# Kernel optimization log

Measured on AMD Instinct MI355X. Metric: run time of the kernel, lower is better.

The kernel has to match this reference:

```python
import jax, jax.numpy as jnp
import numpy as np

LSH_NUM_PROJS = 7
BLOCK_SIZE = 256
SAMPLE_SIZE = 256
B, H, N, D = 2, 16, 8192, 64


def _gray_perm(num_projs):
    # Gray-code ordering so adjacent hash buckets differ by 1 bit (AngularLSH.perm)
    a = np.array([0, 1], dtype=np.int32)
    for _ in range(num_projs - 1):
        a = np.concatenate([a, a[::-1] + a.shape[0]])
    return a

_PERM = jnp.asarray(_gray_perm(LSH_NUM_PROJS))
_ENC = 2 ** jnp.arange(LSH_NUM_PROJS, dtype=jnp.int32)


def lsh_hash(x, proj_dir):
    # x: [b,h,n,d], proj_dir: [1,1,d,r] -> bucket ids [b,h,n]
    proj = jnp.einsum('...nd,...dr->...nr', x, proj_dir)
    bits = (proj > 0).astype(jnp.int32)
    return _PERM[(bits * _ENC).sum(-1)]


def gather_seq(x, idx):
    # x: [b,h,n,d], idx: [b,h,s] -> [b,h,s,d]
    return jnp.take_along_axis(x, idx[..., None], axis=2)


def setup_inputs() -> dict:
    key = jax.random.key(0)
    kq, kk, kv, kp, ks = jax.random.split(key, 5)
    query = jax.random.normal(kq, (B, H, N, D), dtype=jnp.float32)
    key_t = jax.random.normal(kk, (B, H, N, D), dtype=jnp.float32)
    value = jax.random.normal(kv, (B, H, N, D), dtype=jnp.float32)
    proj_dir = jax.random.normal(kp, (1, 1, D, LSH_NUM_PROJS), dtype=jnp.float32)
    # uniform sampling WITHOUT replacement per (b,h), like torch.multinomial
    skeys = jax.random.split(ks, B * H)
    sampled_set = jax.vmap(lambda k: jax.random.permutation(k, N)[:SAMPLE_SIZE])(skeys)
    sampled_set = sampled_set.reshape(B, H, SAMPLE_SIZE).astype(jnp.int32)
    return {'query': query, 'key': key_t, 'value': value,
            'proj_dir': proj_dir, 'sampled_set': sampled_set}


def reference(query, key, value, proj_dir, sampled_set):
    b, h, n, d = query.shape
    scale = d ** -0.5
    neg_min = jnp.finfo(query.dtype).min

    # ---- 1. LSH-sort queries and keys (stable sort on bucket ids) ----
    q_idx = jnp.argsort(lsh_hash(query, proj_dir), axis=2, stable=True)
    k_idx = jnp.argsort(lsh_hash(key, proj_dir), axis=2, stable=True)
    q_idx_inv = jnp.argsort(q_idx, axis=2, stable=True)
    q_s = gather_seq(query, q_idx)
    k_s = gather_seq(key, k_idx)
    v_s = gather_seq(value, k_idx)

    # ---- 2. block-diagonal exact attention on sorted order ----
    nb = n // BLOCK_SIZE               # n divisible by block_size (8192/256=32)
    qbs = n // nb                       # query_block_size == 256 here
    qb = q_s.reshape(b, h, nb, qbs, d)
    kb = k_s.reshape(b, h, nb, BLOCK_SIZE, d)
    vb = v_s.reshape(b, h, nb, BLOCK_SIZE, d)
    qk = jnp.einsum('bhnqd,bhnkd->bhnqk', qb, kb) * scale
    lse_blk = jax.nn.logsumexp(qk, axis=-1, keepdims=True)
    attn_blk = jnp.einsum('bhnqk,bhnkd->bhnqd', jnp.exp(qk - lse_blk), vb)
    attn_blk = attn_blk.reshape(b, h, n, d)
    lse_blk = lse_blk.reshape(b, h, n, 1)

    # ---- 3. sampled-column residual attention ----
    k_sub = gather_seq(k_s, sampled_set)   # [b,h,S,d]
    v_sub = gather_seq(v_s, sampled_set)
    row_blk = (jnp.arange(n) // qbs)[None, None, :, None]            # [1,1,n,1]
    col_blk = (sampled_set // BLOCK_SIZE)[:, :, None, :]             # [b,h,1,S]
    in_block = row_blk == col_blk                                    # [b,h,n,S]
    sampled_cnt = SAMPLE_SIZE - in_block.sum(-1, keepdims=True).astype(query.dtype)
    bias = in_block.astype(query.dtype) * neg_min                    # mask double-counted cols
    qk_r = jnp.einsum('bhnd,bhsd->bhns', q_s, k_sub) * scale + bias
    lse_r = jax.nn.logsumexp(qk_r, axis=-1, keepdims=True)
    attn_r = jnp.einsum('bhns,bhsd->bhnd', jnp.exp(qk_r - lse_r), v_sub)
    # approximate_unsampled: rescale sampled mass to stand in for all
    # (n - block_size) out-of-block columns
    lse_r = lse_r + jnp.log((n - BLOCK_SIZE) / sampled_cnt)

    # ---- 4. combine the two attention estimates (add_self_attentions) ----
    lse = jnp.logaddexp(lse_blk, lse_r)
    c = jnp.exp(lse_blk - lse)
    attn = c * attn_blk + (1.0 - c) * attn_r

    # ---- 5. un-sort rows back to original query order ----
    attn = gather_seq(attn, q_idx_inv)
    return attn
```

## Files before the change

kernel.cpp:

```cpp
#include <hip/hip_runtime.h>
#include <math.h>

#define BH    32
#define NSEQ  8192
#define DDIM  64
#define NPROJ 7
#define BLK   256
#define NB    32
#define PITCH 72
#define PPITCH 40
#define LOG2E 1.44269504f
#define SC2   0.180336881f

typedef _Float16 v8h __attribute__((ext_vector_type(8)));
typedef _Float16 v4h __attribute__((ext_vector_type(4)));
typedef float    v4f __attribute__((ext_vector_type(4)));

__global__ __launch_bounds__(256) void hash_kernel(
        const float* __restrict__ query,
        const float* __restrict__ key,
        const float* __restrict__ proj,
        int* __restrict__ buckets)
{
    const float* x = (blockIdx.y == 0) ? query : key;
    const int t = threadIdx.x;
    const int row = blockIdx.x * 256 + t;

    __shared__ double pdd[64 * NPROJ];
    for (int i = t; i < 64 * NPROJ; i += 256) pdd[i] = (double)proj[i];
    __syncthreads();

    const float4* rp = (const float4*)(x + (size_t)row * DDIM);
    double acc[NPROJ];
    #pragma unroll
    for (int r = 0; r < NPROJ; ++r) acc[r] = 0.0;

    #pragma unroll
    for (int i = 0; i < 16; ++i) {
        float4 v = rp[i];
        float e[4] = {v.x, v.y, v.z, v.w};
        #pragma unroll
        for (int c = 0; c < 4; ++c) {
            double xv = (double)e[c];
            const int d = i * 4 + c;
            #pragma unroll
            for (int r = 0; r < NPROJ; ++r)
                acc[r] += xv * pdd[d * NPROJ + r];
        }
    }
    int code = 0;
    #pragma unroll
    for (int r = 0; r < NPROJ; ++r)
        if (acc[r] > 0.0) code |= (1 << r);
    buckets[(size_t)blockIdx.y * (BH * NSEQ) + row] = code ^ (code >> 1);
}

#define SCNT 258
__global__ __launch_bounds__(256) void sort_kernel(
        const int* __restrict__ buckets,
        int* __restrict__ q_idx,
        int* __restrict__ k_idx)
{
    const int bh = blockIdx.x;
    const int t = threadIdx.x;
    const int lane = t & 63, w = t >> 6;
    const int* b = buckets + (size_t)blockIdx.y * (BH * NSEQ) + (size_t)bh * NSEQ;
    int* out = ((blockIdx.y == 0) ? q_idx : k_idx) + (size_t)bh * NSEQ;

    __shared__ unsigned short cnt[128 * SCNT];
    __shared__ unsigned int partial[256];
    __shared__ unsigned int wsum[4];

    unsigned int* cz = (unsigned int*)cnt;
    for (int i = t; i < 128 * SCNT / 2; i += 256) cz[i] = 0;

    int4 rv[8];
    const int4* b4 = (const int4*)b;
    #pragma unroll
    for (int s = 0; s < 8; ++s) rv[s] = b4[t * 8 + s];
    __syncthreads();

    #pragma unroll
    for (int s = 0; s < 8; ++s) {
        cnt[rv[s].x * SCNT + t]++;
        cnt[rv[s].y * SCNT + t]++;
        cnt[rv[s].z * SCNT + t]++;
        cnt[rv[s].w * SCNT + t]++;
    }
    __syncthreads();

    const int v0 = t >> 1, tt0 = (t & 1) * 128;
    {
        unsigned int s = 0;
        for (int j = 0; j < 128; ++j) s += cnt[v0 * SCNT + tt0 + j];
        partial[t] = s;
    }
    __syncthreads();

    unsigned int chunkoff;
    {
        unsigned int x = partial[t], own = x;
        #pragma unroll
        for (int d = 1; d < 64; d <<= 1) {
            unsigned int y = __shfl_up(x, d);
            if (lane >= d) x += y;
        }
        if (lane == 63) wsum[w] = x;
        __syncthreads();
        unsigned int wb0 = 0;
        if (w == 1) wb0 = wsum[0];
        else if (w == 2) wb0 = wsum[0] + wsum[1];
        else if (w == 3) wb0 = wsum[0] + wsum[1] + wsum[2];
        chunkoff = x - own + wb0;
    }

    {
        unsigned int s = chunkoff;
        for (int j = 0; j < 128; ++j) {
            unsigned short c = cnt[v0 * SCNT + tt0 + j];
            cnt[v0 * SCNT + tt0 + j] = (unsigned short)s;
            s += c;
        }
    }
    __syncthreads();

    const int i0 = t * 32;
    #pragma unroll
    for (int s = 0; s < 8; ++s) {
        int4 q = rv[s];
        int j4 = i0 + s * 4;
        { unsigned short p = cnt[q.x * SCNT + t]++; out[p] = j4 + 0; }
        { unsigned short p = cnt[q.y * SCNT + t]++; out[p] = j4 + 1; }
        { unsigned short p = cnt[q.z * SCNT + t]++; out[p] = j4 + 2; }
        { unsigned short p = cnt[q.w * SCNT + t]++; out[p] = j4 + 3; }
    }
}

__global__ __launch_bounds__(256, 2) void attn_kernel(
        const float* __restrict__ query,
        const float* __restrict__ key,
        const float* __restrict__ value,
        const int* __restrict__ sampled,
        const int* __restrict__ q_idx,
        const int* __restrict__ k_idx,
        float* __restrict__ outp)
{
    const int qb = blockIdx.x;
    const int bh = blockIdx.y;
    const int t  = threadIdx.x;
    const int w    = t >> 6;
    const int lane = t & 63;
    const int quad = lane >> 4;
    const int nrow = lane & 15;

    __shared__ __align__(16) unsigned char smem[38912];
    _Float16* Kc = (_Float16*)smem;
    _Float16* Vt = (_Float16*)(smem + 9216);
    _Float16* Pb = (_Float16*)(smem + 18432);
    _Float16* Ob = (_Float16*)smem;
    __shared__ int s_row[512];
    __shared__ __align__(16) float lb[512];
    __shared__ int s_qi[256];
    __shared__ int wb[4];

    const size_t bhN = (size_t)bh * NSEQ;

    {
        s_qi[t] = q_idx[bhN + qb * BLK + t];
        s_row[t] = k_idx[bhN + qb * BLK + t];
        int ss = sampled[bh * BLK + t];
        s_row[256 + t] = k_idx[bhN + ss];
        int sb = ss >> 8;
        unsigned long long mk = __ballot(sb == qb);
        if (lane == 0) wb[w] = __popcll(mk);
        __syncthreads();
        int cnt_in = wb[0] + wb[1] + wb[2] + wb[3];
        float J = __logf((float)(NSEQ - BLK) / (float)(BLK - cnt_in));
        lb[t] = -6.0f * LOG2E;
        lb[256 + t] = (sb == qb) ? -3.0e4f : (J - 6.0f) * LOG2E;
    }

    const int kr_r = t >> 2, kr_seg = t & 3;
    const int vs_kq = t & 15, vs_dg = t >> 4;

    float4 kreg0, kreg1, kreg2, kreg3;
    float4 vreg0, vreg1, vreg2, vreg3;

    #define ISSUE_LOADS(ch_) do {                                              \
        int krow_ = s_row[(ch_) * 64 + kr_r];                                  \
        const float4* kp_ = (const float4*)(key + (bhN + (size_t)krow_) * DDIM \
                                            + kr_seg * 16);                    \
        kreg0 = kp_[0]; kreg1 = kp_[1]; kreg2 = kp_[2]; kreg3 = kp_[3];        \
        int vr0_ = s_row[(ch_) * 64 + vs_kq * 4 + 0];                          \
        int vr1_ = s_row[(ch_) * 64 + vs_kq * 4 + 1];                          \
        int vr2_ = s_row[(ch_) * 64 + vs_kq * 4 + 2];                          \
        int vr3_ = s_row[(ch_) * 64 + vs_kq * 4 + 3];                          \
        vreg0 = *(const float4*)(value + (bhN + (size_t)vr0_) * DDIM + vs_dg * 4); \
        vreg1 = *(const float4*)(value + (bhN + (size_t)vr1_) * DDIM + vs_dg * 4); \
        vreg2 = *(const float4*)(value + (bhN + (size_t)vr2_) * DDIM + vs_dg * 4); \
        vreg3 = *(const float4*)(value + (bhN + (size_t)vr3_) * DDIM + vs_dg * 4); \
    } while (0)

    ISSUE_LOADS(0);

    v8h qf[4][2];
    #pragma unroll
    for (int ni = 0; ni < 4; ++ni) {
        int qi = s_qi[w * 64 + ni * 16 + nrow];
        const float* qp = query + (bhN + (size_t)qi) * DDIM;
        #pragma unroll
        for (int k2 = 0; k2 < 2; ++k2) {
            const float4* q4 = (const float4*)(qp + k2 * 32 + quad * 8);
            float4 a = q4[0], bvec = q4[1];
            v8h h;
            h[0]=(_Float16)a.x; h[1]=(_Float16)a.y; h[2]=(_Float16)a.z; h[3]=(_Float16)a.w;
            h[4]=(_Float16)bvec.x; h[5]=(_Float16)bvec.y; h[6]=(_Float16)bvec.z; h[7]=(_Float16)bvec.w;
            qf[ni][k2] = h;
        }
    }

    v4f Oacc[4][4];
    float l_part[4];
    #pragma unroll
    for (int ni = 0; ni < 4; ++ni) {
        l_part[ni] = 0.f;
        #pragma unroll
        for (int mi2 = 0; mi2 < 4; ++mi2) Oacc[mi2][ni] = (v4f){0.f, 0.f, 0.f, 0.f};
    }
    _Float16* Pw = Pb + w * 64 * PPITCH;

    #pragma unroll 1
    for (int ch = 0; ch < 8; ++ch) {
        __syncthreads();
        {
            v8h h0, h1;
            h0[0]=(_Float16)kreg0.x; h0[1]=(_Float16)kreg0.y; h0[2]=(_Float16)kreg0.z; h0[3]=(_Float16)kreg0.w;
            h0[4]=(_Float16)kreg1.x; h0[5]=(_Float16)kreg1.y; h0[6]=(_Float16)kreg1.z; h0[7]=(_Float16)kreg1.w;
            h1[0]=(_Float16)kreg2.x; h1[1]=(_Float16)kreg2.y; h1[2]=(_Float16)kreg2.z; h1[3]=(_Float16)kreg2.w;
            h1[4]=(_Float16)kreg3.x; h1[5]=(_Float16)kreg3.y; h1[6]=(_Float16)kreg3.z; h1[7]=(_Float16)kreg3.w;
            *(v8h*)&Kc[kr_r * PITCH + kr_seg * 16] = h0;
            *(v8h*)&Kc[kr_r * PITCH + kr_seg * 16 + 8] = h1;
        }
        {
            v4h h0, h1, h2, h3;
            h0[0]=(_Float16)vreg0.x; h0[1]=(_Float16)vreg1.x; h0[2]=(_Float16)vreg2.x; h0[3]=(_Float16)vreg3.x;
            h1[0]=(_Float16)vreg0.y; h1[1]=(_Float16)vreg1.y; h1[2]=(_Float16)vreg2.y; h1[3]=(_Float16)vreg3.y;
            h2[0]=(_Float16)vreg0.z; h2[1]=(_Float16)vreg1.z; h2[2]=(_Float16)vreg2.z; h2[3]=(_Float16)vreg3.z;
            h3[0]=(_Float16)vreg0.w; h3[1]=(_Float16)vreg1.w; h3[2]=(_Float16)vreg2.w; h3[3]=(_Float16)vreg3.w;
            *(v4h*)&Vt[(vs_dg * 4 + 0) * PITCH + vs_kq * 4] = h0;
            *(v4h*)&Vt[(vs_dg * 4 + 1) * PITCH + vs_kq * 4] = h1;
            *(v4h*)&Vt[(vs_dg * 4 + 2) * PITCH + vs_kq * 4] = h2;
            *(v4h*)&Vt[(vs_dg * 4 + 3) * PITCH + vs_kq * 4] = h3;
        }
        if (ch < 7) ISSUE_LOADS(ch + 1);
        __syncthreads();

        #pragma unroll
        for (int ks = 0; ks < 2; ++ks) {
            #pragma unroll
            for (int mi = 0; mi < 2; ++mi) {
                v4f bb = *(const v4f*)&lb[ch * 64 + ks * 32 + mi * 16 + quad * 4];
                const int krow = ks * 32 + mi * 16 + nrow;
                v8h ka0 = *(const v8h*)&Kc[krow * PITCH + quad * 8];
                v8h ka1 = *(const v8h*)&Kc[krow * PITCH + 32 + quad * 8];
                #pragma unroll
                for (int ni = 0; ni < 4; ++ni) {
                    v4f S = (v4f){0.f, 0.f, 0.f, 0.f};
                    S = __builtin_amdgcn_mfma_f32_16x16x32_f16(ka0, qf[ni][0], S, 0, 0, 0);
                    S = __builtin_amdgcn_mfma_f32_16x16x32_f16(ka1, qf[ni][1], S, 0, 0, 0);
                    v4h ph;
                    #pragma unroll
                    for (int r = 0; r < 4; ++r)
                        ph[r] = (_Float16)__builtin_amdgcn_exp2f(fmaf(S[r], SC2, bb[r]));
                    l_part[ni] += ((float)ph[0] + (float)ph[1])
                                + ((float)ph[2] + (float)ph[3]);
                    *(v4h*)&Pw[(ni * 16 + nrow) * PPITCH + mi * 16 + quad * 4] = ph;
                }
            }
            v8h pbv[4];
            #pragma unroll
            for (int ni = 0; ni < 4; ++ni)
                pbv[ni] = *(const v8h*)&Pw[(ni * 16 + nrow) * PPITCH + quad * 8];
            __builtin_amdgcn_s_setprio(1);
            #pragma unroll
            for (int mi2 = 0; mi2 < 4; ++mi2) {
                v8h va = *(const v8h*)&Vt[(mi2 * 16 + nrow) * PITCH + ks * 32 + quad * 8];
                #pragma unroll
                for (int ni = 0; ni < 4; ++ni)
                    Oacc[mi2][ni] = __builtin_amdgcn_mfma_f32_16x16x32_f16(va, pbv[ni], Oacc[mi2][ni], 0, 0, 0);
            }
            __builtin_amdgcn_s_setprio(0);
        }
    }

    __syncthreads();
    #pragma unroll
    for (int ni = 0; ni < 4; ++ni) {
        float l = l_part[ni];
        l += __shfl_xor(l, 16);
        l += __shfl_xor(l, 32);
        float inv = 1.0f / l;
        #pragma unroll
        for (int mi2 = 0; mi2 < 4; ++mi2) {
            v4h h;
            #pragma unroll
            for (int r = 0; r < 4; ++r)
                h[r] = (_Float16)(Oacc[mi2][ni][r] * inv);
            *(v4h*)&Ob[(w * 64 + ni * 16 + nrow) * PITCH + mi2 * 16 + quad * 4] = h;
        }
    }
    __syncthreads();

    #pragma unroll
    for (int p = 0; p < 4; ++p) {
        int row = p * 64 + (t >> 2);
        int seg = t & 3;
        const _Float16* src = &Ob[row * PITCH + seg * 16];
        v8h x0 = *(const v8h*)src;
        v8h x1 = *(const v8h*)(src + 8);
        int qi = s_qi[row];
        float4* op = (float4*)(outp + (bhN + (size_t)qi) * DDIM + seg * 16);
        op[0] = make_float4((float)x0[0], (float)x0[1], (float)x0[2], (float)x0[3]);
        op[1] = make_float4((float)x0[4], (float)x0[5], (float)x0[6], (float)x0[7]);
        op[2] = make_float4((float)x1[0], (float)x1[1], (float)x1[2], (float)x1[3]);
        op[3] = make_float4((float)x1[4], (float)x1[5], (float)x1[6], (float)x1[7]);
    }
}

extern "C" void kernel_launch(void* const* d_in, const int* in_sizes, int n_in,
                              void* d_out, int out_size, void* d_ws, size_t ws_size,
                              hipStream_t stream) {
    (void)in_sizes; (void)n_in; (void)out_size; (void)ws_size;
    const float* query = (const float*)d_in[0];
    const float* key   = (const float*)d_in[1];
    const float* value = (const float*)d_in[2];
    const float* proj  = (const float*)d_in[3];
    const int* sampled = (const int*)d_in[4];
    float* out = (float*)d_out;

    int* buckets = (int*)d_ws;
    int* q_idx   = buckets + 2 * BH * NSEQ;
    int* k_idx   = q_idx + BH * NSEQ;

    hash_kernel<<<dim3(BH * NSEQ / 256, 2), 256, 0, stream>>>(query, key, proj, buckets);
    sort_kernel<<<dim3(BH, 2), 256, 0, stream>>>(buckets, q_idx, k_idx);
    attn_kernel<<<dim3(NB, BH), 256, 0, stream>>>(query, key, value, sampled,
                                                  q_idx, k_idx, out);
}
```

Baseline: 290.3 us.

## Split attention block across eight waves with fewer query rows each

Doubles the attention block size from 256 to 512 threads so each wave handles 32 query rows instead of 64. The K/V staging work is redistributed so each thread loads half as much. The goal is fewer registers per thread and more waves to hide latency. The tighter launch bound (512 threads, 4 blocks) may force register spills, and each wave now does less MFMA work per shared-memory read.

```diff
diff --git a/kernel.cpp b/kernel.cpp
--- a/kernel.cpp
+++ b/kernel.cpp
@@ -136,7 +136,7 @@
     }
 }
 
-__global__ __launch_bounds__(256, 2) void attn_kernel(
+__global__ __launch_bounds__(512, 4) void attn_kernel(
         const float* __restrict__ query,
         const float* __restrict__ key,
         const float* __restrict__ value,
@@ -165,48 +165,51 @@
 
     const size_t bhN = (size_t)bh * NSEQ;
 
-    {
+    int ss = 0, sb = 0;
+    if (t < 256) {
         s_qi[t] = q_idx[bhN + qb * BLK + t];
         s_row[t] = k_idx[bhN + qb * BLK + t];
-        int ss = sampled[bh * BLK + t];
+        ss = sampled[bh * BLK + t];
         s_row[256 + t] = k_idx[bhN + ss];
-        int sb = ss >> 8;
+        sb = ss >> 8;
         unsigned long long mk = __ballot(sb == qb);
         if (lane == 0) wb[w] = __popcll(mk);
-        __syncthreads();
+    }
+    __syncthreads();
+    if (t < 256) {
         int cnt_in = wb[0] + wb[1] + wb[2] + wb[3];
         float J = __logf((float)(NSEQ - BLK) / (float)(BLK - cnt_in));
         lb[t] = -6.0f * LOG2E;
         lb[256 + t] = (sb == qb) ? -3.0e4f : (J - 6.0f) * LOG2E;
     }
 
-    const int kr_r = t >> 2, kr_seg = t & 3;
+    const int kr_r = t >> 3, kr_seg = t & 7;
     const int vs_kq = t & 15, vs_dg = t >> 4;
 
-    float4 kreg0, kreg1, kreg2, kreg3;
-    float4 vreg0, vreg1, vreg2, vreg3;
+    float4 kreg0, kreg1;
+    float2 vreg0, vreg1, vreg2, vreg3;
 
     #define ISSUE_LOADS(ch_) do {                                              \
         int krow_ = s_row[(ch_) * 64 + kr_r];                                  \
         const float4* kp_ = (const float4*)(key + (bhN + (size_t)krow_) * DDIM \
-                                            + kr_seg * 16);                    \
-        kreg0 = kp_[0]; kreg1 = kp_[1]; kreg2 = kp_[2]; kreg3 = kp_[3];        \
+                                            + kr_seg * 8);                     \
+        kreg0 = kp_[0]; kreg1 = kp_[1];                                        \
         int vr0_ = s_row[(ch_) * 64 + vs_kq * 4 + 0];                          \
         int vr1_ = s_row[(ch_) * 64 + vs_kq * 4 + 1];                          \
         int vr2_ = s_row[(ch_) * 64 + vs_kq * 4 + 2];                          \
         int vr3_ = s_row[(ch_) * 64 + vs_kq * 4 + 3];                          \
-        vreg0 = *(const float4*)(value + (bhN + (size_t)vr0_) * DDIM + vs_dg * 4); \
-        vreg1 = *(const float4*)(value + (bhN + (size_t)vr1_) * DDIM + vs_dg * 4); \
-        vreg2 = *(const float4*)(value + (bhN + (size_t)vr2_) * DDIM + vs_dg * 4); \
-        vreg3 = *(const float4*)(value + (bhN + (size_t)vr3_) * DDIM + vs_dg * 4); \
+        vreg0 = *(const float2*)(value + (bhN + (size_t)vr0_) * DDIM + vs_dg * 2); \
+        vreg1 = *(const float2*)(value + (bhN + (size_t)vr1_) * DDIM + vs_dg * 2); \
+        vreg2 = *(const float2*)(value + (bhN + (size_t)vr2_) * DDIM + vs_dg * 2); \
+        vreg3 = *(const float2*)(value + (bhN + (size_t)vr3_) * DDIM + vs_dg * 2); \
     } while (0)
 
     ISSUE_LOADS(0);
 
-    v8h qf[4][2];
-    #pragma unroll
-    for (int ni = 0; ni < 4; ++ni) {
-        int qi = s_qi[w * 64 + ni * 16 + nrow];
+    v8h qf[2][2];
+    #pragma unroll
+    for (int ni = 0; ni < 2; ++ni) {
+        int qi = s_qi[w * 32 + ni * 16 + nrow];
         const float* qp = query + (bhN + (size_t)qi) * DDIM;
         #pragma unroll
         for (int k2 = 0; k2 < 2; ++k2) {
@@ -219,38 +222,31 @@
         }
     }
 
-    v4f Oacc[4][4];
-    float l_part[4];
-    #pragma unroll
-    for (int ni = 0; ni < 4; ++ni) {
+    v4f Oacc[4][2];
+    float l_part[2];
+    #pragma unroll
+    for (int ni = 0; ni < 2; ++ni) {
         l_part[ni] = 0.f;
         #pragma unroll
         for (int mi2 = 0; mi2 < 4; ++mi2) Oacc[mi2][ni] = (v4f){0.f, 0.f, 0.f, 0.f};
     }
-    _Float16* Pw = Pb + w * 64 * PPITCH;
+    _Float16* Pw = Pb + w * 32 * PPITCH;
 
     #pragma unroll 1
     for (int ch = 0; ch < 8; ++ch) {
         __syncthreads();
         {
-            v8h h0, h1;
+            v8h h0;
             h0[0]=(_Float16)kreg0.x; h0[1]=(_Float16)kreg0.y; h0[2]=(_Float16)kreg0.z; h0[3]=(_Float16)kreg0.w;
             h0[4]=(_Float16)kreg1.x; h0[5]=(_Float16)kreg1.y; h0[6]=(_Float16)kreg1.z; h0[7]=(_Float16)kreg1.w;
-            h1[0]=(_Float16)kreg2.x; h1[1]=(_Float16)kreg2.y; h1[2]=(_Float16)kreg2.z; h1[3]=(_Float16)kreg2.w;
-            h1[4]=(_Float16)kreg3.x; h1[5]=(_Float16)kreg3.y; h1[6]=(_Float16)kreg3.z; h1[7]=(_Float16)kreg3.w;
-            *(v8h*)&Kc[kr_r * PITCH + kr_seg * 16] = h0;
-            *(v8h*)&Kc[kr_r * PITCH + kr_seg * 16 + 8] = h1;
+            *(v8h*)&Kc[kr_r * PITCH + kr_seg * 8] = h0;
         }
         {
-            v4h h0, h1, h2, h3;
+            v4h h0, h1;
             h0[0]=(_Float16)vreg0.x; h0[1]=(_Float16)vreg1.x; h0[2]=(_Float16)vreg2.x; h0[3]=(_Float16)vreg3.x;
             h1[0]=(_Float16)vreg0.y; h1[1]=(_Float16)vreg1.y; h1[2]=(_Float16)vreg2.y; h1[3]=(_Float16)vreg3.y;
-            h2[0]=(_Float16)vreg0.z; h2[1]=(_Float16)vreg1.z; h2[2]=(_Float16)vreg2.z; h2[3]=(_Float16)vreg3.z;
-            h3[0]=(_Float16)vreg0.w; h3[1]=(_Float16)vreg1.w; h3[2]=(_Float16)vreg2.w; h3[3]=(_Float16)vreg3.w;
-            *(v4h*)&Vt[(vs_dg * 4 + 0) * PITCH + vs_kq * 4] = h0;
-            *(v4h*)&Vt[(vs_dg * 4 + 1) * PITCH + vs_kq * 4] = h1;
-            *(v4h*)&Vt[(vs_dg * 4 + 2) * PITCH + vs_kq * 4] = h2;
-            *(v4h*)&Vt[(vs_dg * 4 + 3) * PITCH + vs_kq * 4] = h3;
+            *(v4h*)&Vt[(vs_dg * 2 + 0) * PITCH + vs_kq * 4] = h0;
+            *(v4h*)&Vt[(vs_dg * 2 + 1) * PITCH + vs_kq * 4] = h1;
         }
         if (ch < 7) ISSUE_LOADS(ch + 1);
         __syncthreads();
@@ -264,7 +260,7 @@
                 v8h ka0 = *(const v8h*)&Kc[krow * PITCH + quad * 8];
                 v8h ka1 = *(const v8h*)&Kc[krow * PITCH + 32 + quad * 8];
                 #pragma unroll
-                for (int ni = 0; ni < 4; ++ni) {
+                for (int ni = 0; ni < 2; ++ni) {
                     v4f S = (v4f){0.f, 0.f, 0.f, 0.f};
                     S = __builtin_amdgcn_mfma_f32_16x16x32_f16(ka0, qf[ni][0], S, 0, 0, 0);
                     S = __builtin_amdgcn_mfma_f32_16x16x32_f16(ka1, qf[ni][1], S, 0, 0, 0);
@@ -277,16 +273,16 @@
                     *(v4h*)&Pw[(ni * 16 + nrow) * PPITCH + mi * 16 + quad * 4] = ph;
                 }
             }
-            v8h pbv[4];
-            #pragma unroll
-            for (int ni = 0; ni < 4; ++ni)
+            v8h pbv[2];
+            #pragma unroll
+            for (int ni = 0; ni < 2; ++ni)
                 pbv[ni] = *(const v8h*)&Pw[(ni * 16 + nrow) * PPITCH + quad * 8];
             __builtin_amdgcn_s_setprio(1);
             #pragma unroll
             for (int mi2 = 0; mi2 < 4; ++mi2) {
                 v8h va = *(const v8h*)&Vt[(mi2 * 16 + nrow) * PITCH + ks * 32 + quad * 8];
                 #pragma unroll
-                for (int ni = 0; ni < 4; ++ni)
+                for (int ni = 0; ni < 2; ++ni)
                     Oacc[mi2][ni] = __builtin_amdgcn_mfma_f32_16x16x32_f16(va, pbv[ni], Oacc[mi2][ni], 0, 0, 0);
             }
             __builtin_amdgcn_s_setprio(0);
@@ -295,7 +291,7 @@
 
     __syncthreads();
     #pragma unroll
-    for (int ni = 0; ni < 4; ++ni) {
+    for (int ni = 0; ni < 2; ++ni) {
         float l = l_part[ni];
         l += __shfl_xor(l, 16);
         l += __shfl_xor(l, 32);
@@ -306,14 +302,14 @@
             #pragma unroll
             for (int r = 0; r < 4; ++r)
                 h[r] = (_Float16)(Oacc[mi2][ni][r] * inv);
-            *(v4h*)&Ob[(w * 64 + ni * 16 + nrow) * PITCH + mi2 * 16 + quad * 4] = h;
-        }
-    }
-    __syncthreads();
-
-    #pragma unroll
-    for (int p = 0; p < 4; ++p) {
-        int row = p * 64 + (t >> 2);
+            *(v4h*)&Ob[(w * 32 + ni * 16 + nrow) * PITCH + mi2 * 16 + quad * 4] = h;
+        }
+    }
+    __syncthreads();
+
+    #pragma unroll
+    for (int p = 0; p < 2; ++p) {
+        int row = p * 128 + (t >> 2);
         int seg = t & 3;
         const _Float16* src = &Ob[row * PITCH + seg * 16];
         v8h x0 = *(const v8h*)src;
@@ -344,6 +340,6 @@
 
     hash_kernel<<<dim3(BH * NSEQ / 256, 2), 256, 0, stream>>>(query, key, proj, buckets);
     sort_kernel<<<dim3(BH, 2), 256, 0, stream>>>(buckets, q_idx, k_idx);
-    attn_kernel<<<dim3(NB, BH), 256, 0, stream>>>(query, key, value, sampled,
+    attn_kernel<<<dim3(NB, BH), 512, 0, stream>>>(query, key, value, sampled,
                                                   q_idx, k_idx, out);
 }
```

After: 292.3 us. About the same (+0.7%).
